# Kernel tuning notes

Measured on AMD Instinct MI355X. Metric: run time of the kernel, lower is better.

The kernel has to match this reference:

```python
import jax, jax.numpy as jnp
import numpy as np

B, IN_SHAPE, EXP_SHAPE, HID, NB_CLASSES = 64, 10000, 53, 1500, 2048


def setup_inputs() -> dict:
    key = jax.random.key(0)
    ks = jax.random.split(key, 8)
    gos = jax.random.uniform(ks[0], (B, IN_SHAPE), dtype=jnp.float32)
    exp_x = jax.random.uniform(ks[1], (B, EXP_SHAPE), dtype=jnp.float32)
    # FlatModel params (torch Linear: y = x @ W.T + b; store pre-transposed)
    W1 = jax.random.normal(ks[2], (IN_SHAPE, HID), dtype=jnp.float32) * (1.0 / np.sqrt(IN_SHAPE))
    b1 = jnp.zeros((HID,), dtype=jnp.float32)
    W2 = jax.random.normal(ks[3], (HID + EXP_SHAPE, NB_CLASSES), dtype=jnp.float32) * (1.0 / np.sqrt(HID + EXP_SHAPE))
    b2 = jnp.zeros((NB_CLASSES,), dtype=jnp.float32)
    # HPO adjacency (non-trainable buffer in the original; values in [0,1))
    hpo_matrix = jax.random.uniform(ks[4], (NB_CLASSES, NB_CLASSES), dtype=jnp.float32)
    return {"gos": gos, "exp_x": exp_x, "W1": W1, "b1": b1, "W2": W2, "b2": b2, "hpo_matrix": hpo_matrix}


def reference(gos, exp_x, W1, b1, W2, b2, hpo_matrix):
    # FlatModel (eval mode: dropout is identity). torch F.gelu default = exact erf gelu.
    h = jax.nn.gelu(gos @ W1 + b1, approximate=False)          # (B, HID)
    x = jnp.concatenate([h, exp_x], axis=1)                     # (B, HID+EXP)
    flat = jax.nn.sigmoid(x @ W2 + b2)                          # (B, C)
    # HPOLayer + permute + MaxPool1d(C): out[b,j] = max_i flat[b,j] * M[i,j]
    out = jnp.max(flat[:, None, :] * hpo_matrix[None, :, :], axis=1)  # (B, C)
    return out
```

## Files before the change

### kernel.cpp

```cpp
#include <hip/hip_runtime.h>
#include <math.h>


#define B64 64
#define IN_SH 10000
#define EXP_SH 53
#define HID 1500
#define NPAD1 1536
#define NBC 2048
#define K2 1553
#define KS1 20
#define KST1 16
#define KS2 13
#define KST2 4
#define NSTEP 52
#define CMCH 32
#define ACC1 (NPAD1 * 64)
#define ACC2 (NBC * 64)

using short8  = __attribute__((ext_vector_type(8))) short;
using floatx4 = __attribute__((ext_vector_type(4))) float;
using uintx4  = __attribute__((ext_vector_type(4))) unsigned int;

__device__ __forceinline__ unsigned short f2bf(float f) {
    unsigned u = __float_as_uint(f);
    u += 0x7fffu + ((u >> 16) & 1u);
    return (unsigned short)(u >> 16);
}

typedef __attribute__((address_space(3))) void lds_v;
typedef __attribute__((address_space(1))) const void glb_v;
__device__ __forceinline__ void gll16(const float* g, float* l) {
    __builtin_amdgcn_global_load_lds((glb_v*)g, (lds_v*)l, 16, 0, 0);
}

#define WVS(n) asm volatile("s_waitcnt vmcnt(" #n ")" ::: "memory")
template<int N> __device__ __forceinline__ void waitv() {
    if constexpr (N >= 20)      WVS(20);
    else if constexpr (N >= 16) WVS(16);
    else if constexpr (N >= 14) WVS(14);
    else if constexpr (N >= 12) WVS(12);
    else if constexpr (N >= 10) WVS(10);
    else if constexpr (N >= 8)  WVS(8);
    else                        WVS(6);
}

constexpr int after_ops(int KS, int st) {
    int n = 0;
    if (st < 4) {
        n += 2 * (3 - st) + 8;
        for (int k = 0; k < st; k++)
            n += (k + 4 < KS ? 2 : 0) + (k + 2 < KS ? 4 : 0);
    } else {
        n += (st - 2 < KS ? 4 : 0);
        for (int k = st - 3; k < st; k++)
            n += (k + 4 < KS ? 2 : 0) + (k + 2 < KS ? 4 : 0);
    }
    return n;
}

template<int KS, int ST>
__device__ __forceinline__ void gstep(
    const float* __restrict__ W, const unsigned short* __restrict__ bf,
    float* __restrict__ ldsw, floatx4 (&acc)[4], uintx4 (&bv)[3][4],
    unsigned wbase, unsigned stepInc, unsigned halfInc, unsigned maxoff,
    int q, int l15)
{
    if constexpr (ST < KS) {
        constexpr int AO = after_ops(KS, ST);
        waitv<(AO > 6 ? AO - 6 : 0)>();
        const float* lb = ldsw + (ST & 3) * 512;
        short8 af;
        #pragma unroll
        for (int j = 0; j < 8; j++)
            af[j] = (short)f2bf(lb[(q * 8 + j) * 16 + l15]);
        if constexpr (ST + 4 < KS) {
            unsigned o0 = wbase + (unsigned)(ST + 4) * stepInc;
            unsigned o1 = o0 + halfInc;
            if (o0 > maxoff) o0 = maxoff;
            if (o1 > maxoff) o1 = maxoff;
            gll16(W + o0, ldsw + ((ST + 4) & 3) * 512);
            gll16(W + o1, ldsw + ((ST + 4) & 3) * 512 + 256);
        }
        if constexpr (ST + 2 < KS) {
            #pragma unroll
            for (int s = 0; s < 4; s++)
                bv[(ST + 2) % 3][s] =
                    *(const uintx4*)(bf + (size_t)((ST + 2) * 4 + s) * 512);
        }
        #pragma unroll
        for (int s = 0; s < 4; s++) {
            short8 b8 = __builtin_bit_cast(short8, bv[ST % 3][s]);
            acc[s] = __builtin_amdgcn_mfma_f32_16x16x32_bf16(af, b8, acc[s], 0, 0, 0);
        }
        gstep<KS, ST + 1>(W, bf, ldsw, acc, bv, wbase, stepInc, halfInc, maxoff, q, l15);
    }
}

template<int KS>
__device__ __forceinline__ void gemm_wave2(
    const float* __restrict__ W, const unsigned short* __restrict__ Bfc,
    float* __restrict__ pbuf, int ldw, unsigned maxoff, int n0, int k0,
    int lane, float* __restrict__ ldsw)
{
    const int q = lane >> 4, l15 = lane & 15;
    const int r = lane >> 2, c4 = (lane & 3) * 4;
    unsigned wbase = (unsigned)((k0 + r) * ldw + n0 + c4);
    const unsigned stepInc = 32u * (unsigned)ldw;
    const unsigned halfInc = 16u * (unsigned)ldw;

    #pragma unroll
    for (int st = 0; st < 4; st++) {
        unsigned o0 = wbase + (unsigned)st * stepInc;
        unsigned o1 = o0 + halfInc;
        if (o0 > maxoff) o0 = maxoff;
        if (o1 > maxoff) o1 = maxoff;
        gll16(W + o0, ldsw + (st & 3) * 512);
        gll16(W + o1, ldsw + (st & 3) * 512 + 256);
    }
    const unsigned short* bf = Bfc + (size_t)lane * 8;
    uintx4 bv[3][4];
    #pragma unroll
    for (int k = 0; k < 2; k++) {
        #pragma unroll
        for (int s = 0; s < 4; s++)
            bv[k][s] = *(const uintx4*)(bf + (size_t)(k * 4 + s) * 512);
    }
    floatx4 acc[4];
    #pragma unroll
    for (int s = 0; s < 4; s++) acc[s] = (floatx4){0.f, 0.f, 0.f, 0.f};

    gstep<KS, 0>(W, bf, ldsw, acc, bv, wbase, stepInc, halfInc, maxoff, q, l15);

    int nrow = n0 + q * 4;
    #pragma unroll
    for (int s = 0; s < 4; s++) {
        #pragma unroll
        for (int rr = 0; rr < 4; rr++)
            pbuf[(size_t)(nrow + rr) * 64 + s * 16 + l15] = acc[s][rr];
    }
}

__global__ __launch_bounds__(256) void prep_k(const float* __restrict__ g,
                                              unsigned short* __restrict__ gosBf) {
    int t    = blockIdx.x * 256 + threadIdx.x;
    int lane = t & 63;
    int sgrp = (t >> 6) & 3;
    int step = t >> 8;
    int q    = lane >> 4;
    int l15  = lane & 15;
    int b    = sgrp * 16 + l15;
    int k0   = step * 32 + q * 8;
    const float* p = g + (size_t)b * IN_SH + k0;
    unsigned int o[4];
    #pragma unroll
    for (int i = 0; i < 4; i++) {
        float lo = (k0 + 2 * i     < IN_SH) ? p[2 * i]     : 0.f;
        float hi = (k0 + 2 * i + 1 < IN_SH) ? p[2 * i + 1] : 0.f;
        o[i] = (unsigned)f2bf(lo) | ((unsigned)f2bf(hi) << 16);
    }
    uintx4 v; v.x = o[0]; v.y = o[1]; v.z = o[2]; v.w = o[3];
    *(uintx4*)(gosBf + (size_t)t * 8) = v;
}

__global__ __launch_bounds__(256, 4) void gemm1_k(
    const float* __restrict__ W1, const unsigned short* __restrict__ gosBf,
    float* __restrict__ hpre_p, const float* __restrict__ M, float* __restrict__ cm)
{
    __shared__ float lds[4 * 2048];
    int bi = blockIdx.x;
    if (bi < 256) {
        int j  = (bi & 7) * 256 + threadIdx.x;
        int i0 = (bi >> 3) * 64;
        float m = 0.0f;
        #pragma unroll 16
        for (int i = i0; i < i0 + 64; i++)
            m = fmaxf(m, M[(size_t)i * NBC + j]);
        cm[(bi >> 3) * NBC + j] = m;
    } else {
        int gb  = bi - 256;
        int bx  = gb % 24;
        int by  = gb / 24;
        int wid = threadIdx.x >> 6;
        gemm_wave2<KST1>(W1, gosBf + (size_t)by * (KST1 * 4) * 512,
                         hpre_p + (size_t)by * ACC1, HID,
                         (unsigned)(IN_SH * HID - 4),
                         bx * 64 + wid * 16, by * (KST1 * 32),
                         threadIdx.x & 63, lds + wid * 2048);
    }
}

__global__ __launch_bounds__(256, 4) void gemm2_k(
    const float* __restrict__ W2, const unsigned short* __restrict__ Xf,
    float* __restrict__ logits_p)
{
    __shared__ float lds[4 * 2048];
    int wid = threadIdx.x >> 6;
    gemm_wave2<KST2>(W2, Xf + (size_t)blockIdx.y * (KST2 * 4) * 512,
                     logits_p + (size_t)blockIdx.y * ACC2, NBC,
                     (unsigned)(K2 * NBC - 4),
                     blockIdx.x * 64 + wid * 16, blockIdx.y * (KST2 * 32),
                     threadIdx.x & 63, lds + wid * 2048);
}

__global__ __launch_bounds__(256) void combine1(
    const float* __restrict__ hpre_p, const float* __restrict__ b1,
    const float* __restrict__ expx, unsigned short* __restrict__ Xf,
    const float* __restrict__ cm, float* __restrict__ cmr)
{
    int bi = blockIdx.x;
    if (bi < 208) {
        int idx = bi * 256 + threadIdx.x;
        int b   = idx & 63;
        int n0  = (idx >> 6) * 2;
        float v[2];
        #pragma unroll
        for (int e = 0; e < 2; e++) {
            int n = n0 + e;
            float x = 0.f;
            if (n < HID) {
                const float* p = hpre_p + (size_t)n * 64 + b;
                float a0 = 0.f, a1 = 0.f, a2 = 0.f, a3 = 0.f;
                #pragma unroll
                for (int ks = 0; ks < KS1; ks += 4) {
                    a0 += p[(size_t)ks * ACC1];
                    a1 += p[(size_t)(ks + 1) * ACC1];
                    a2 += p[(size_t)(ks + 2) * ACC1];
                    a3 += p[(size_t)(ks + 3) * ACC1];
                }
                float s = b1[n] + ((a0 + a1) + (a2 + a3));
                x = 0.5f * s * (1.0f + erff(s * 0.70710678118654752f));
            } else if (n < HID + EXP_SH) {
                x = expx[b * EXP_SH + (n - HID)];
            }
            v[e] = x;
        }
        unsigned o = (unsigned)f2bf(v[0]) | ((unsigned)f2bf(v[1]) << 16);
        int step = n0 >> 5, w = n0 & 31, q = w >> 3, j = w & 7;
        int sgrp = b >> 4, l15 = b & 15;
        size_t tq = (size_t)(step * 4 + sgrp) * 64 + q * 16 + l15;
        *(unsigned*)(Xf + tq * 8 + j) = o;
    } else {
        int j = (bi - 208) * 256 + threadIdx.x;
        float m = 0.f;
        #pragma unroll
        for (int c = 0; c < CMCH; c++) m = fmaxf(m, cm[c * NBC + j]);
        cmr[j] = m;
    }
}

__global__ __launch_bounds__(256) void final_k(
    const float* __restrict__ logits_p, const float* __restrict__ b2,
    const float* __restrict__ cmr, float* __restrict__ out)
{
    __shared__ float lds[32 * 65];
    int j0  = blockIdx.x * 32;
    int tid = threadIdx.x;
    #pragma unroll
    for (int e = 0; e < 8; e++) {
        int lin = e * 256 + tid;
        int jj  = lin >> 6;
        int b   = lin & 63;
        int j   = j0 + jj;
        float s = b2[j];
        const float* p = logits_p + (size_t)j * 64 + b;
        #pragma unroll
        for (int ks = 0; ks < KS2; ks++)
            s += p[(size_t)ks * ACC2];
        float sig = 1.0f / (1.0f + expf(-s));
        lds[jj * 65 + b] = sig * cmr[j];
    }
    __syncthreads();
    #pragma unroll
    for (int e = 0; e < 8; e++) {
        int lin = e * 256 + tid;
        int b   = lin >> 5;
        int jj  = lin & 31;
        out[(size_t)b * NBC + j0 + jj] = lds[jj * 65 + b];
    }
}

extern "C" void kernel_launch(void* const* d_in, const int* in_sizes, int n_in,
                              void* d_out, int out_size, void* d_ws, size_t ws_size,
                              hipStream_t stream) {
    const float* gos  = (const float*)d_in[0];
    const float* expx = (const float*)d_in[1];
    const float* W1   = (const float*)d_in[2];
    const float* b1   = (const float*)d_in[3];
    const float* W2   = (const float*)d_in[4];
    const float* b2   = (const float*)d_in[5];
    const float* hpo  = (const float*)d_in[6];
    float* out = (float*)d_out;

    char* ws = (char*)d_ws;
    unsigned short* gosBf = (unsigned short*)ws;
    unsigned short* Xf    = (unsigned short*)(ws + 1310720);
    float* cm       = (float*)(ws + 1523712);
    float* cmr      = (float*)(ws + 1785856);
    float* hpre_p   = (float*)(ws + 1794048);
    float* logits_p = (float*)(ws + 9658368);

    prep_k<<<320, 256, 0, stream>>>(gos, gosBf);

    gemm1_k<<<256 + 24 * KS1, 256, 0, stream>>>(W1, gosBf, hpre_p, hpo, cm);

    combine1<<<216, 256, 0, stream>>>(hpre_p, b1, expx, Xf, cm, cmr);

    gemm2_k<<<dim3(32, KS2), 256, 0, stream>>>(W2, Xf, logits_p);

    final_k<<<64, 256, 0, stream>>>(logits_p, b2, cmr, out);
}
```

Measured before the change: 153.7 us.

## Fuse GEMM2 with sigmoid epilogue, drop split-K, move column max into prep

GEMM2 now runs without split-K: each of 32 blocks walks the full K=1553 through a deeper 8-stage LDS ring. Bias, sigmoid and the column-max scaling are applied in its epilogue, so the separate final kernel and the partial-logit buffer go away. The HPO column-max work moves from gemm1 into the prep kernel, and gemm1 blocks get a swizzled index mapping. This saves one launch and the partial-sum traffic, but gemm2 drops to 32 blocks each running a 52-step serial loop, which may leave most CUs idle.

```diff
diff --git a/kernel.cpp b/kernel.cpp
--- a/kernel.cpp
+++ b/kernel.cpp
@@ -11,12 +11,9 @@
 #define K2 1553
 #define KS1 20
 #define KST1 16
-#define KS2 13
-#define KST2 4
-#define NSTEP 52
+#define KST2 52
 #define CMCH 32
 #define ACC1 (NPAD1 * 64)
-#define ACC2 (NBC * 64)
 
 using short8  = __attribute__((ext_vector_type(8))) short;
 using floatx4 = __attribute__((ext_vector_type(4))) float;
@@ -36,30 +33,38 @@
 
 #define WVS(n) asm volatile("s_waitcnt vmcnt(" #n ")" ::: "memory")
 template<int N> __device__ __forceinline__ void waitv() {
-    if constexpr (N >= 20)      WVS(20);
+    if constexpr (N >= 44)      WVS(44);
+    else if constexpr (N >= 40) WVS(40);
+    else if constexpr (N >= 36) WVS(36);
+    else if constexpr (N >= 32) WVS(32);
+    else if constexpr (N >= 28) WVS(28);
+    else if constexpr (N >= 24) WVS(24);
+    else if constexpr (N >= 20) WVS(20);
     else if constexpr (N >= 16) WVS(16);
-    else if constexpr (N >= 14) WVS(14);
     else if constexpr (N >= 12) WVS(12);
     else if constexpr (N >= 10) WVS(10);
     else if constexpr (N >= 8)  WVS(8);
-    else                        WVS(6);
-}
-
-constexpr int after_ops(int KS, int st) {
+    else if constexpr (N >= 6)  WVS(6);
+    else if constexpr (N >= 4)  WVS(4);
+    else if constexpr (N >= 2)  WVS(2);
+    else                        WVS(0);
+}
+
+constexpr int after_ops(int KS, int RING, int st) {
     int n = 0;
-    if (st < 4) {
-        n += 2 * (3 - st) + 8;
+    if (st < RING) {
+        n += 2 * (RING - 1 - st) + 8;
         for (int k = 0; k < st; k++)
-            n += (k + 4 < KS ? 2 : 0) + (k + 2 < KS ? 4 : 0);
+            n += (k + RING < KS ? 2 : 0) + (k + 2 < KS ? 4 : 0);
     } else {
-        n += (st - 2 < KS ? 4 : 0);
-        for (int k = st - 3; k < st; k++)
-            n += (k + 4 < KS ? 2 : 0) + (k + 2 < KS ? 4 : 0);
+        n += (st - RING + 2 < KS ? 4 : 0);
+        for (int k = st - RING + 1; k < st; k++)
+            n += (k + RING < KS ? 2 : 0) + (k + 2 < KS ? 4 : 0);
     }
     return n;
 }
 
-template<int KS, int ST>
+template<int KS, int RING, int ST>
 __device__ __forceinline__ void gstep(
     const float* __restrict__ W, const unsigned short* __restrict__ bf,
     float* __restrict__ ldsw, floatx4 (&acc)[4], uintx4 (&bv)[3][4],
@@ -67,20 +72,20 @@
     int q, int l15)
 {
     if constexpr (ST < KS) {
-        constexpr int AO = after_ops(KS, ST);
+        constexpr int AO = after_ops(KS, RING, ST);
         waitv<(AO > 6 ? AO - 6 : 0)>();
-        const float* lb = ldsw + (ST & 3) * 512;
+        const float* lb = ldsw + (ST % RING) * 512;
         short8 af;
         #pragma unroll
         for (int j = 0; j < 8; j++)
             af[j] = (short)f2bf(lb[(q * 8 + j) * 16 + l15]);
-        if constexpr (ST + 4 < KS) {
-            unsigned o0 = wbase + (unsigned)(ST + 4) * stepInc;
+        if constexpr (ST + RING < KS) {
+            unsigned o0 = wbase + (unsigned)(ST + RING) * stepInc;
             unsigned o1 = o0 + halfInc;
             if (o0 > maxoff) o0 = maxoff;
             if (o1 > maxoff) o1 = maxoff;
-            gll16(W + o0, ldsw + ((ST + 4) & 3) * 512);
-            gll16(W + o1, ldsw + ((ST + 4) & 3) * 512 + 256);
+            gll16(W + o0, ldsw + ((ST + RING) % RING) * 512);
+            gll16(W + o1, ldsw + ((ST + RING) % RING) * 512 + 256);
         }
         if constexpr (ST + 2 < KS) {
             #pragma unroll
@@ -93,14 +98,15 @@
             short8 b8 = __builtin_bit_cast(short8, bv[ST % 3][s]);
             acc[s] = __builtin_amdgcn_mfma_f32_16x16x32_bf16(af, b8, acc[s], 0, 0, 0);
         }
-        gstep<KS, ST + 1>(W, bf, ldsw, acc, bv, wbase, stepInc, halfInc, maxoff, q, l15);
-    }
-}
-
-template<int KS>
-__device__ __forceinline__ void gemm_wave2(
+        gstep<KS, RING, ST + 1>(W, bf, ldsw, acc, bv, wbase, stepInc, halfInc,
+                                maxoff, q, l15);
+    }
+}
+
+template<int KS, int RING>
+__device__ __forceinline__ void gemm_ring(
     const float* __restrict__ W, const unsigned short* __restrict__ Bfc,
-    float* __restrict__ pbuf, int ldw, unsigned maxoff, int n0, int k0,
+    floatx4 (&acc)[4], int ldw, unsigned maxoff, int n0, int k0,
     int lane, float* __restrict__ ldsw)
 {
     const int q = lane >> 4, l15 = lane & 15;
@@ -110,13 +116,13 @@
     const unsigned halfInc = 16u * (unsigned)ldw;
 
     #pragma unroll
-    for (int st = 0; st < 4; st++) {
+    for (int st = 0; st < RING; st++) {
         unsigned o0 = wbase + (unsigned)st * stepInc;
         unsigned o1 = o0 + halfInc;
         if (o0 > maxoff) o0 = maxoff;
         if (o1 > maxoff) o1 = maxoff;
-        gll16(W + o0, ldsw + (st & 3) * 512);
-        gll16(W + o1, ldsw + (st & 3) * 512 + 256);
+        gll16(W + o0, ldsw + st * 512);
+        gll16(W + o1, ldsw + st * 512 + 256);
     }
     const unsigned short* bf = Bfc + (size_t)lane * 8;
     uintx4 bv[3][4];
@@ -126,81 +132,73 @@
         for (int s = 0; s < 4; s++)
             bv[k][s] = *(const uintx4*)(bf + (size_t)(k * 4 + s) * 512);
     }
-    floatx4 acc[4];
     #pragma unroll
     for (int s = 0; s < 4; s++) acc[s] = (floatx4){0.f, 0.f, 0.f, 0.f};
 
-    gstep<KS, 0>(W, bf, ldsw, acc, bv, wbase, stepInc, halfInc, maxoff, q, l15);
-
-    int nrow = n0 + q * 4;
-    #pragma unroll
-    for (int s = 0; s < 4; s++) {
-        #pragma unroll
-        for (int rr = 0; rr < 4; rr++)
-            pbuf[(size_t)(nrow + rr) * 64 + s * 16 + l15] = acc[s][rr];
-    }
-}
-
-__global__ __launch_bounds__(256) void prep_k(const float* __restrict__ g,
-                                              unsigned short* __restrict__ gosBf) {
-    int t    = blockIdx.x * 256 + threadIdx.x;
-    int lane = t & 63;
-    int sgrp = (t >> 6) & 3;
-    int step = t >> 8;
-    int q    = lane >> 4;
-    int l15  = lane & 15;
-    int b    = sgrp * 16 + l15;
-    int k0   = step * 32 + q * 8;
-    const float* p = g + (size_t)b * IN_SH + k0;
-    unsigned int o[4];
-    #pragma unroll
-    for (int i = 0; i < 4; i++) {
-        float lo = (k0 + 2 * i     < IN_SH) ? p[2 * i]     : 0.f;
-        float hi = (k0 + 2 * i + 1 < IN_SH) ? p[2 * i + 1] : 0.f;
-        o[i] = (unsigned)f2bf(lo) | ((unsigned)f2bf(hi) << 16);
-    }
-    uintx4 v; v.x = o[0]; v.y = o[1]; v.z = o[2]; v.w = o[3];
-    *(uintx4*)(gosBf + (size_t)t * 8) = v;
-}
-
-__global__ __launch_bounds__(256, 4) void gemm1_k(
-    const float* __restrict__ W1, const unsigned short* __restrict__ gosBf,
-    float* __restrict__ hpre_p, const float* __restrict__ M, float* __restrict__ cm)
-{
-    __shared__ float lds[4 * 2048];
+    gstep<KS, RING, 0>(W, bf, ldsw, acc, bv, wbase, stepInc, halfInc, maxoff, q, l15);
+}
+
+__global__ __launch_bounds__(256) void prep_k(
+    const float* __restrict__ g, unsigned short* __restrict__ gosBf,
+    const float* __restrict__ M, float* __restrict__ cm)
+{
     int bi = blockIdx.x;
-    if (bi < 256) {
-        int j  = (bi & 7) * 256 + threadIdx.x;
-        int i0 = (bi >> 3) * 64;
+    if (bi < 320) {
+        int t    = bi * 256 + threadIdx.x;
+        int lane = t & 63;
+        int sgrp = (t >> 6) & 3;
+        int step = t >> 8;
+        int q    = lane >> 4;
+        int l15  = lane & 15;
+        int b    = sgrp * 16 + l15;
+        int k0   = step * 32 + q * 8;
+        const float* p = g + (size_t)b * IN_SH + k0;
+        unsigned int o[4];
+        #pragma unroll
+        for (int i = 0; i < 4; i++) {
+            float lo = (k0 + 2 * i     < IN_SH) ? p[2 * i]     : 0.f;
+            float hi = (k0 + 2 * i + 1 < IN_SH) ? p[2 * i + 1] : 0.f;
+            o[i] = (unsigned)f2bf(lo) | ((unsigned)f2bf(hi) << 16);
+        }
+        uintx4 v; v.x = o[0]; v.y = o[1]; v.z = o[2]; v.w = o[3];
+        *(uintx4*)(gosBf + (size_t)t * 8) = v;
+    } else {
+        int u  = bi - 320;
+        int j  = (u & 7) * 256 + threadIdx.x;
+        int i0 = (u >> 3) * 64;
         float m = 0.0f;
         #pragma unroll 16
         for (int i = i0; i < i0 + 64; i++)
             m = fmaxf(m, M[(size_t)i * NBC + j]);
-        cm[(bi >> 3) * NBC + j] = m;
-    } else {
-        int gb  = bi - 256;
-        int bx  = gb % 24;
-        int by  = gb / 24;
-        int wid = threadIdx.x >> 6;
-        gemm_wave2<KST1>(W1, gosBf + (size_t)by * (KST1 * 4) * 512,
-                         hpre_p + (size_t)by * ACC1, HID,
-                         (unsigned)(IN_SH * HID - 4),
-                         bx * 64 + wid * 16, by * (KST1 * 32),
-                         threadIdx.x & 63, lds + wid * 2048);
-    }
-}
-
-__global__ __launch_bounds__(256, 4) void gemm2_k(
-    const float* __restrict__ W2, const unsigned short* __restrict__ Xf,
-    float* __restrict__ logits_p)
+        cm[(u >> 3) * NBC + j] = m;
+    }
+}
+
+__global__ __launch_bounds__(256, 4) void gemm1_k(
+    const float* __restrict__ W1, const unsigned short* __restrict__ gosBf,
+    float* __restrict__ hpre_p)
 {
     __shared__ float lds[4 * 2048];
+    int bi  = blockIdx.x;
+    int swz = (bi & 7) * 60 + (bi >> 3);
+    int bx  = swz % 24;
+    int by  = swz / 24;
     int wid = threadIdx.x >> 6;
-    gemm_wave2<KST2>(W2, Xf + (size_t)blockIdx.y * (KST2 * 4) * 512,
-                     logits_p + (size_t)blockIdx.y * ACC2, NBC,
-                     (unsigned)(K2 * NBC - 4),
-                     blockIdx.x * 64 + wid * 16, blockIdx.y * (KST2 * 32),
-                     threadIdx.x & 63, lds + wid * 2048);
+    int lane = threadIdx.x & 63;
+    floatx4 acc[4];
+    gemm_ring<KST1, 4>(W1, gosBf + (size_t)by * (KST1 * 4) * 512, acc, HID,
+                       (unsigned)(IN_SH * HID - 4),
+                       bx * 64 + wid * 16, by * (KST1 * 32),
+                       lane, lds + wid * 2048);
+    int q = lane >> 4, l15 = lane & 15;
+    int nrow = bx * 64 + wid * 16 + q * 4;
+    float* pbuf = hpre_p + (size_t)by * ACC1;
+    #pragma unroll
+    for (int s = 0; s < 4; s++) {
+        #pragma unroll
+        for (int rr = 0; rr < 4; rr++)
+            pbuf[(size_t)(nrow + rr) * 64 + s * 16 + l15] = acc[s][rr];
+    }
 }
 
 __global__ __launch_bounds__(256) void combine1(
@@ -249,33 +247,36 @@
     }
 }
 
-__global__ __launch_bounds__(256) void final_k(
-    const float* __restrict__ logits_p, const float* __restrict__ b2,
-    const float* __restrict__ cmr, float* __restrict__ out)
-{
-    __shared__ float lds[32 * 65];
-    int j0  = blockIdx.x * 32;
-    int tid = threadIdx.x;
-    #pragma unroll
-    for (int e = 0; e < 8; e++) {
+__global__ __launch_bounds__(256) void gemm2_k(
+    const float* __restrict__ W2, const unsigned short* __restrict__ Xf,
+    const float* __restrict__ b2, const float* __restrict__ cmr,
+    float* __restrict__ out)
+{
+    __shared__ float lds[4 * 4096];
+    int tid = threadIdx.x, lane = tid & 63, wid = tid >> 6;
+    int j0 = blockIdx.x * 64;
+    int n0 = j0 + wid * 16;
+    floatx4 acc[4];
+    gemm_ring<KST2, 8>(W2, Xf, acc, NBC, (unsigned)(K2 * NBC - 4),
+                       n0, 0, lane, lds + wid * 4096);
+    int q = lane >> 4, l15 = lane & 15;
+    __syncthreads();
+    #pragma unroll
+    for (int s = 0; s < 4; s++) {
+        #pragma unroll
+        for (int rr = 0; rr < 4; rr++) {
+            int j = n0 + q * 4 + rr;
+            float v = acc[s][rr] + b2[j];
+            v = (1.0f / (1.0f + expf(-v))) * cmr[j];
+            lds[(wid * 16 + q * 4 + rr) * 65 + s * 16 + l15] = v;
+        }
+    }
+    __syncthreads();
+    #pragma unroll
+    for (int e = 0; e < 16; e++) {
         int lin = e * 256 + tid;
-        int jj  = lin >> 6;
-        int b   = lin & 63;
-        int j   = j0 + jj;
-        float s = b2[j];
-        const float* p = logits_p + (size_t)j * 64 + b;
-        #pragma unroll
-        for (int ks = 0; ks < KS2; ks++)
-            s += p[(size_t)ks * ACC2];
-        float sig = 1.0f / (1.0f + expf(-s));
-        lds[jj * 65 + b] = sig * cmr[j];
-    }
-    __syncthreads();
-    #pragma unroll
-    for (int e = 0; e < 8; e++) {
-        int lin = e * 256 + tid;
-        int b   = lin >> 5;
-        int jj  = lin & 31;
+        int b   = lin >> 6;
+        int jj  = lin & 63;
         out[(size_t)b * NBC + j0 + jj] = lds[jj * 65 + b];
     }
 }
@@ -295,18 +296,15 @@
     char* ws = (char*)d_ws;
     unsigned short* gosBf = (unsigned short*)ws;
     unsigned short* Xf    = (unsigned short*)(ws + 1310720);
-    float* cm       = (float*)(ws + 1523712);
-    float* cmr      = (float*)(ws + 1785856);
-    float* hpre_p   = (float*)(ws + 1794048);
-    float* logits_p = (float*)(ws + 9658368);
-
-    prep_k<<<320, 256, 0, stream>>>(gos, gosBf);
-
-    gemm1_k<<<256 + 24 * KS1, 256, 0, stream>>>(W1, gosBf, hpre_p, hpo, cm);
+    float* cm     = (float*)(ws + 1523712);
+    float* cmr    = (float*)(ws + 1785856);
+    float* hpre_p = (float*)(ws + 1794048);
+
+    prep_k<<<576, 256, 0, stream>>>(gos, gosBf, hpo, cm);
+
+    gemm1_k<<<480, 256, 0, stream>>>(W1, gosBf, hpre_p);
 
     combine1<<<216, 256, 0, stream>>>(hpre_p, b1, expx, Xf, cm, cmr);
 
-    gemm2_k<<<dim3(32, KS2), 256, 0, stream>>>(W2, Xf, logits_p);
-
-    final_k<<<64, 256, 0, stream>>>(logits_p, b2, cmr, out);
-}
+    gemm2_k<<<32, 256, 0, stream>>>(W2, Xf, b2, cmr, out);
+}
```

After: 174.1 us. 1.13x slower.
